# Kernel optimization log

Measured on AMD Instinct MI355X. Metric: run time of the kernel, lower is better.

Reference implementation:

```python
import jax, jax.numpy as jnp
import numpy as np

K = 3          # kernel size (implied by 18/27 offset channels)
PAD = 1
STRIDE = 1


def setup_inputs() -> dict:
    key = jax.random.key(0)
    k0, k1, k2 = jax.random.split(key, 3)
    B, C, H, W = 4, 256, 64, 64
    Cout = 256
    x = jax.random.normal(k0, (B, C, H, W), jnp.float32)
    # offset/mask predicting conv: 18 offset + 9 mask channels (deform_group=1)
    w_off = jax.random.normal(k1, (27, C, K, K), jnp.float32) * 0.01
    b_off = jnp.zeros((27,), jnp.float32)
    # main deformable conv weight (bias=False)
    w = jax.random.normal(k2, (Cout, C, K, K), jnp.float32) * 0.05
    return {"x": x, "w_off": w_off, "b_off": b_off, "w": w}


def _modulated_dcn(x, w_off, b_off, w):
    B, C, H, W = x.shape
    KK = K * K
    # regular conv predicting offsets (+ mask)
    om = jax.lax.conv_general_dilated(
        x, w_off, (STRIDE, STRIDE), [(PAD, PAD), (PAD, PAD)],
        dimension_numbers=("NCHW", "OIHW", "NCHW")) + b_off[None, :, None, None]
    Ho, Wo = om.shape[2], om.shape[3]
    # channel layout: interleaved (dy, dx) per kernel tap, then 9 mask channels
    off = om[:, :2 * KK].reshape(B, KK, 2, Ho, Wo)
    mask = jax.nn.sigmoid(om[:, 2 * KK:3 * KK])            # (B, KK, Ho, Wo)

    ky, kx = jnp.meshgrid(jnp.arange(K), jnp.arange(K), indexing="ij")
    base_y = (jnp.arange(Ho) * STRIDE - PAD)[:, None]       # (Ho, 1)
    base_x = (jnp.arange(Wo) * STRIDE - PAD)[None, :]       # (1, Wo)
    # sampling positions p = p0 + pn + offset, shape (B, KK, Ho, Wo)
    py = base_y[None, None] + ky.reshape(KK)[None, :, None, None] + off[:, :, 0]
    px = base_x[None, None] + kx.reshape(KK)[None, :, None, None] + off[:, :, 1]

    y0f = jnp.floor(py)
    x0f = jnp.floor(px)
    ly = py - y0f
    lx = px - x0f
    y0 = y0f.astype(jnp.int32)
    x0 = x0f.astype(jnp.int32)

    xf = x.reshape(B, C, H * W)

    def samp(yi, xi):
        valid = ((yi >= 0) & (yi < H) & (xi >= 0) & (xi < W)).astype(x.dtype)
        idx = jnp.clip(yi, 0, H - 1) * W + jnp.clip(xi, 0, W - 1)
        v = jnp.take_along_axis(xf, idx.reshape(B, 1, -1), axis=2)
        return v.reshape(B, C, KK, Ho, Wo) * valid[:, None]

    # bilinear interpolation with zero padding outside the image
    v = (samp(y0,     x0    ) * ((1 - ly) * (1 - lx))[:, None]
         + samp(y0,     x0 + 1) * ((1 - ly) * lx)[:, None]
         + samp(y0 + 1, x0    ) * (ly * (1 - lx))[:, None]
         + samp(y0 + 1, x0 + 1) * (ly * lx)[:, None])
    v = v * mask[:, None]                                   # modulation
    # conv as contraction over (Cin, KK)
    return jnp.einsum("bckhw,ock->bohw", v, w.reshape(w.shape[0], C, KK))


def reference(x, w_off, b_off, w):
    return _modulated_dcn(x, w_off, b_off, w)
```

## Files before the change

kernel.cpp:

```cpp
#include <hip/hip_runtime.h>
#include <math.h>

#define HH 64
#define WW 64
#define CIN 256
#define COUT 256
#define KKT 9
#define HWSZ 4096
#define VP 260

typedef __bf16  v8bf   __attribute__((ext_vector_type(8)));
typedef float   v4f    __attribute__((ext_vector_type(4)));
typedef short   short8 __attribute__((ext_vector_type(8)));
typedef unsigned short ushort4v __attribute__((ext_vector_type(4)));

__device__ inline unsigned short f2bf(float f) {
    union { float f; unsigned u; } uf; uf.f = f;
    unsigned r = uf.u + 0x7fff + ((uf.u >> 16) & 1);
    return (unsigned short)(r >> 16);
}
__device__ inline float bf2f(unsigned short u) {
    union { unsigned u; float f; } uf; uf.u = ((unsigned)u) << 16;
    return uf.f;
}

__global__ __launch_bounds__(256) void k_prep_x(const float* __restrict__ x,
                                                unsigned short* __restrict__ x_t) {
    int bh = blockIdx.x;
    int b  = bh >> 6;
    int h  = bh & 63;
    int px  = threadIdx.x & 63;
    int oct = threadIdx.x >> 6;
    const float* xr = x + (((size_t)b * CIN) * HH + h) * WW;
    unsigned short* orow = x_t + (((size_t)bh) * WW + px) * CIN;
    for (int g = 0; g < 8; g++) {
        int cb = g * 32 + oct * 8;
        unsigned short v[8];
#pragma unroll
        for (int j = 0; j < 8; j++)
            v[j] = f2bf(xr[(size_t)(cb + j) * HWSZ + px]);
        *(short8*)(orow + cb) = *(short8*)v;
    }
}

__global__ __launch_bounds__(256) void k_prep_wts(const float* __restrict__ w,
                                                  const float* __restrict__ w_off,
                                                  unsigned short* __restrict__ wprep,
                                                  unsigned short* __restrict__ woffp) {
    if (blockIdx.x < 256) {
        int o = blockIdx.x;
        for (int ck = threadIdx.x; ck < 2304; ck += 256) {
            float v = w[(size_t)o * 2304 + ck];
            int c  = ck / 9;
            int kk = ck - 9 * c;
            int kp = kk * 256 + c;
            wprep[((size_t)((kp >> 5) * 256 + o)) * 32 + (kp & 31)] = f2bf(v);
        }
    } else {
        int t = blockIdx.x - 256;
#pragma unroll
        for (int i = 0; i < 4; i++) {
            int idx = i * 256 + threadIdx.x;
            int och = idx >> 5;
            int ki  = idx & 31;
            int kp  = t * 32 + ki;
            int kk  = kp >> 8;
            int c   = kp & 255;
            float v = (och < 27) ? w_off[((size_t)och * 256 + c) * 9 + kk] : 0.f;
            woffp[(size_t)t * 1024 + idx] = f2bf(v);
        }
    }
}

__global__ __launch_bounds__(256) void k_off_mfma(const unsigned short* __restrict__ x_t,
                                                  const unsigned short* __restrict__ woffp,
                                                  const float* __restrict__ b_off,
                                                  float* __restrict__ om) {
    int id = blockIdx.x;
    int g  = id & 7, hi = (id >> 3) & 7, b = id >> 6;
    int h  = g * 8 + hi;
    int tid  = threadIdx.x;
    int lane = tid & 63;
    int wv   = tid >> 6;
    int m16  = lane & 15;
    int quad = lane >> 4;

    __shared__ unsigned short s_row[66 * VP];

    v4f acc[2];
    acc[0] = (v4f)(0.f);
    acc[1] = (v4f)(0.f);

    const unsigned short* xb = x_t + (size_t)b * HWSZ * CIN;

    if (tid < 64) {
        int hpx = (tid >> 5) * 65;
        int c8  = (tid & 31) * 8;
        *(short8*)&s_row[hpx * VP + c8] = (short8)0;
    }

    for (int ky = 0; ky < 3; ky++) {
        int y = h + ky - 1;
        __syncthreads();
        if ((unsigned)y < HH) {
            const unsigned short* src = xb + (size_t)y * WW * CIN;
#pragma unroll
            for (int i = 0; i < 8; i++) {
                int u  = i * 256 + tid;
                int px = u >> 5;
                int c8 = (u & 31) * 8;
                *(short8*)&s_row[(px + 1) * VP + c8] = *(const short8*)(src + px * CIN + c8);
            }
        } else {
#pragma unroll
            for (int i = 0; i < 8; i++) {
                int u  = i * 256 + tid;
                int px = u >> 5;
                int c8 = (u & 31) * 8;
                *(short8*)&s_row[(px + 1) * VP + c8] = (short8)0;
            }
        }
        __syncthreads();

#pragma unroll
        for (int kx = 0; kx < 3; kx++) {
            int kk = ky * 3 + kx;
#pragma unroll 4
            for (int ch = 0; ch < 8; ch++) {
                int t = kk * 8 + ch;
                const unsigned short* wp = woffp + (size_t)t * 1024;
                short8 af0 = *(const short8*)(wp + m16 * 32 + quad * 8);
                short8 af1 = *(const short8*)(wp + (16 + m16) * 32 + quad * 8);
                short8 bfr = *(const short8*)&s_row[(wv * 16 + m16 + kx) * VP + ch * 32 + quad * 8];
                acc[0] = __builtin_amdgcn_mfma_f32_16x16x32_bf16(
                    __builtin_bit_cast(v8bf, af0), __builtin_bit_cast(v8bf, bfr), acc[0], 0, 0, 0);
                acc[1] = __builtin_amdgcn_mfma_f32_16x16x32_bf16(
                    __builtin_bit_cast(v8bf, af1), __builtin_bit_cast(v8bf, bfr), acc[1], 0, 0, 0);
            }
        }
    }

#pragma unroll
    for (int mt = 0; mt < 2; mt++) {
#pragma unroll
        for (int r = 0; r < 4; r++) {
            int och = mt * 16 + quad * 4 + r;
            if (och < 27)
                om[((size_t)b * 27 + och) * HWSZ + h * WW + wv * 16 + m16] =
                    acc[mt][r] + b_off[och];
        }
    }
}

__global__ __launch_bounds__(512) void k_main(const unsigned short* __restrict__ x_t,
                                              const float* __restrict__ om,
                                              const unsigned short* __restrict__ wprep,
                                              float* __restrict__ out) {
    int id = blockIdx.x;
    int g  = id & 7, hi = (id >> 3) & 7, b = id >> 6;
    int h  = g * 8 + hi;
    int tid  = threadIdx.x;
    int lane = tid & 63;
    int oct  = tid >> 6;
    int m16  = lane & 15;
    int quad = lane >> 4;

    __shared__ int4   s_base[KKT][64];
    __shared__ float4 s_wt  [KKT][64];
    __shared__ unsigned short s_v[64 * VP];

    const float* omb = om + (size_t)b * 27 * HWSZ + h * WW;
    for (int i = tid; i < KKT * 64; i += 512) {
        int kk = i >> 6;
        int p  = i & 63;
        float offy = omb[(size_t)(2 * kk)     * HWSZ + p];
        float offx = omb[(size_t)(2 * kk + 1) * HWSZ + p];
        float mv   = omb[(size_t)(18 + kk)    * HWSZ + p];
        int ky = kk / 3, kx = kk - 3 * (kk / 3);
        float py = (float)(h - 1 + ky) + offy;
        float px = (float)(p - 1 + kx) + offx;
        float y0f = floorf(py);
        float x0f = floorf(px);
        float ly = py - y0f, lx = px - x0f;
        int y0 = (int)y0f, x0 = (int)x0f;
        float m = 1.f / (1.f + __expf(-mv));
        bool yv0 = (unsigned)y0       < HH;
        bool yv1 = (unsigned)(y0 + 1) < HH;
        bool xv0 = (unsigned)x0       < WW;
        bool xv1 = (unsigned)(x0 + 1) < WW;
        int y0c = min(max(y0, 0), HH - 1);
        int y1c = min(max(y0 + 1, 0), HH - 1);
        int x0c = min(max(x0, 0), WW - 1);
        int x1c = min(max(x0 + 1, 0), WW - 1);
        s_base[kk][p] = make_int4((y0c * WW + x0c) * CIN, (y0c * WW + x1c) * CIN,
                                  (y1c * WW + x0c) * CIN, (y1c * WW + x1c) * CIN);
        s_wt[kk][p] = make_float4(
            (yv0 && xv0) ? (1.f - ly) * (1.f - lx) * m : 0.f,
            (yv0 && xv1) ? (1.f - ly) * lx         * m : 0.f,
            (yv1 && xv0) ? ly * (1.f - lx)         * m : 0.f,
            (yv1 && xv1) ? ly * lx                 * m : 0.f);
    }
    __syncthreads();

    v4f acc[2][4];
#pragma unroll
    for (int mt = 0; mt < 2; mt++)
#pragma unroll
        for (int nt = 0; nt < 4; nt++) acc[mt][nt] = (v4f)(0.f);

    const unsigned short* xb = x_t + (size_t)b * HWSZ * CIN;

    for (int kk = 0; kk < KKT; kk++) {
#pragma unroll
        for (int i = 0; i < 8; i++) {
            int px = oct * 8 + i;
            int4   bp = s_base[kk][px];
            float4 wt = s_wt[kk][px];
            const unsigned short* xc = xb + lane * 4;
            ushort4v t0 = *(const ushort4v*)(xc + bp.x);
            ushort4v t1 = *(const ushort4v*)(xc + bp.y);
            ushort4v t2 = *(const ushort4v*)(xc + bp.z);
            ushort4v t3 = *(const ushort4v*)(xc + bp.w);
            unsigned short vv[4];
#pragma unroll
            for (int j = 0; j < 4; j++) {
                float val = wt.x * bf2f(t0[j]) + wt.y * bf2f(t1[j])
                          + wt.z * bf2f(t2[j]) + wt.w * bf2f(t3[j]);
                vv[j] = f2bf(val);
            }
            *(ushort4v*)&s_v[px * VP + lane * 4] = *(ushort4v*)vv;
        }
        __syncthreads();

#pragma unroll 2
        for (int ch = 0; ch < 8; ch++) {
            int t = kk * 8 + ch;
            const unsigned short* wp = wprep + ((size_t)t * 256 + oct * 32) * 32;
            short8 af0 = *(const short8*)(wp + m16 * 32 + quad * 8);
            short8 af1 = *(const short8*)(wp + (16 + m16) * 32 + quad * 8);
            short8 bfr[4];
#pragma unroll
            for (int nt = 0; nt < 4; nt++)
                bfr[nt] = *(const short8*)&s_v[(nt * 16 + m16) * VP + ch * 32 + quad * 8];
#pragma unroll
            for (int nt = 0; nt < 4; nt++) {
                acc[0][nt] = __builtin_amdgcn_mfma_f32_16x16x32_bf16(
                    __builtin_bit_cast(v8bf, af0), __builtin_bit_cast(v8bf, bfr[nt]),
                    acc[0][nt], 0, 0, 0);
                acc[1][nt] = __builtin_amdgcn_mfma_f32_16x16x32_bf16(
                    __builtin_bit_cast(v8bf, af1), __builtin_bit_cast(v8bf, bfr[nt]),
                    acc[1][nt], 0, 0, 0);
            }
        }
        __syncthreads();
    }

    float* ob = out + ((size_t)b * COUT) * HWSZ + h * WW;
#pragma unroll
    for (int mt = 0; mt < 2; mt++)
#pragma unroll
        for (int nt = 0; nt < 4; nt++)
#pragma unroll
            for (int r = 0; r < 4; r++) {
                int o = oct * 32 + mt * 16 + quad * 4 + r;
                ob[(size_t)o * HWSZ + nt * 16 + m16] = acc[mt][nt][r];
            }
}

extern "C" void kernel_launch(void* const* d_in, const int* in_sizes, int n_in,
                              void* d_out, int out_size, void* d_ws, size_t ws_size,
                              hipStream_t stream) {
    const float* x     = (const float*)d_in[0];
    const float* w_off = (const float*)d_in[1];
    const float* b_off = (const float*)d_in[2];
    const float* w     = (const float*)d_in[3];
    float* out = (float*)d_out;

    float* om = (float*)d_ws;
    unsigned short* x_t   = (unsigned short*)(om + 442368);
    unsigned short* wprep = x_t + (size_t)4 * HWSZ * CIN;
    unsigned short* woffp = wprep + 589824;

    hipLaunchKernelGGL(k_prep_x,   dim3(256), dim3(256), 0, stream, x, x_t);
    hipLaunchKernelGGL(k_prep_wts, dim3(328), dim3(256), 0, stream, w, w_off, wprep, woffp);
    hipLaunchKernelGGL(k_off_mfma, dim3(256), dim3(256), 0, stream, x_t, woffp, b_off, om);
    hipLaunchKernelGGL(k_main,     dim3(256), dim3(512), 0, stream, x_t, om, wprep, out);
}
```

Before: 156.6 us.

## Merge prep kernels, split offset conv, and double-buffer main gather with prefetch

Merges the x and weight prep kernels into one launch and stages w through shared memory, so the wprep writes become vectorized and coalesced. The offset conv now runs on 512 blocks, each covering half a row; all three input rows are loaded up front and the channel chunks are split across waves, with a shared-memory reduction at the end. The main kernel double-buffers the sampled tile and prefetches the next tap's gathered values and the next weight fragments into registers, which removes one barrier per tap. This costs more registers and more shared memory.

```diff
diff --git a/kernel.cpp b/kernel.cpp
--- a/kernel.cpp
+++ b/kernel.cpp
@@ -24,43 +24,52 @@
     return uf.f;
 }
 
-__global__ __launch_bounds__(256) void k_prep_x(const float* __restrict__ x,
-                                                unsigned short* __restrict__ x_t) {
-    int bh = blockIdx.x;
-    int b  = bh >> 6;
-    int h  = bh & 63;
-    int px  = threadIdx.x & 63;
-    int oct = threadIdx.x >> 6;
-    const float* xr = x + (((size_t)b * CIN) * HH + h) * WW;
-    unsigned short* orow = x_t + (((size_t)bh) * WW + px) * CIN;
-    for (int g = 0; g < 8; g++) {
-        int cb = g * 32 + oct * 8;
-        unsigned short v[8];
-#pragma unroll
-        for (int j = 0; j < 8; j++)
-            v[j] = f2bf(xr[(size_t)(cb + j) * HWSZ + px]);
-        *(short8*)(orow + cb) = *(short8*)v;
-    }
-}
-
-__global__ __launch_bounds__(256) void k_prep_wts(const float* __restrict__ w,
-                                                  const float* __restrict__ w_off,
-                                                  unsigned short* __restrict__ wprep,
-                                                  unsigned short* __restrict__ woffp) {
-    if (blockIdx.x < 256) {
-        int o = blockIdx.x;
-        for (int ck = threadIdx.x; ck < 2304; ck += 256) {
-            float v = w[(size_t)o * 2304 + ck];
-            int c  = ck / 9;
-            int kk = ck - 9 * c;
-            int kp = kk * 256 + c;
-            wprep[((size_t)((kp >> 5) * 256 + o)) * 32 + (kp & 31)] = f2bf(v);
+__global__ __launch_bounds__(256) void k_prep(const float* __restrict__ x,
+                                              const float* __restrict__ w,
+                                              const float* __restrict__ w_off,
+                                              unsigned short* __restrict__ x_t,
+                                              unsigned short* __restrict__ wprep,
+                                              unsigned short* __restrict__ woffp) {
+    __shared__ float s_w[2304];
+    int id  = blockIdx.x;
+    int tid = threadIdx.x;
+    if (id < 256) {
+        int b  = id >> 6;
+        int h  = id & 63;
+        int px  = tid & 63;
+        int oct = tid >> 6;
+        const float* xr = x + (((size_t)b * CIN) * HH + h) * WW;
+        unsigned short* orow = x_t + (((size_t)id) * WW + px) * CIN;
+        for (int g = 0; g < 8; g++) {
+            int cb = g * 32 + oct * 8;
+            unsigned short v[8];
+#pragma unroll
+            for (int j = 0; j < 8; j++)
+                v[j] = f2bf(xr[(size_t)(cb + j) * HWSZ + px]);
+            *(short8*)(orow + cb) = *(short8*)v;
+        }
+    } else if (id < 512) {
+        int o = id - 256;
+        for (int i = tid; i < 2304; i += 256) s_w[i] = w[(size_t)o * 2304 + i];
+        __syncthreads();
+        for (int u = tid; u < 576; u += 256) {
+            int t  = u >> 3;
+            int kq = u & 7;
+            unsigned short v[4];
+#pragma unroll
+            for (int j = 0; j < 4; j++) {
+                int kp = t * 32 + kq * 4 + j;
+                int kk = kp >> 8;
+                int c  = kp & 255;
+                v[j] = f2bf(s_w[c * 9 + kk]);
+            }
+            *(ushort4v*)&wprep[((size_t)(t * 256 + o)) * 32 + kq * 4] = *(ushort4v*)v;
         }
     } else {
-        int t = blockIdx.x - 256;
+        int t = id - 512;
 #pragma unroll
         for (int i = 0; i < 4; i++) {
-            int idx = i * 256 + threadIdx.x;
+            int idx = i * 256 + tid;
             int och = idx >> 5;
             int ki  = idx & 31;
             int kp  = t * 32 + ki;
@@ -76,62 +85,57 @@
                                                   const unsigned short* __restrict__ woffp,
                                                   const float* __restrict__ b_off,
                                                   float* __restrict__ om) {
-    int id = blockIdx.x;
-    int g  = id & 7, hi = (id >> 3) & 7, b = id >> 6;
-    int h  = g * 8 + hi;
+    int id    = blockIdx.x;
+    int g     = id & 7;
+    int phalf = (id >> 3) & 1;
+    int hi    = (id >> 4) & 7;
+    int b     = id >> 7;
+    int h     = g * 8 + hi;
+    int p0    = phalf * 32;
     int tid  = threadIdx.x;
     int lane = tid & 63;
     int wv   = tid >> 6;
+    int g2   = wv >> 1;
+    int ntw  = wv & 1;
     int m16  = lane & 15;
     int quad = lane >> 4;
 
-    __shared__ unsigned short s_row[66 * VP];
+    __shared__ unsigned short s_row[3 * 34 * VP];
+    __shared__ float s_red[2][32][33];
+
+    const unsigned short* xb = x_t + (size_t)b * HWSZ * CIN;
+
+    for (int u = tid; u < 3 * 1088; u += 256) {
+        int row = u / 1088;
+        int rem = u - row * 1088;
+        int px  = rem >> 5;
+        int c8  = (rem & 31) * 8;
+        int y   = h + row - 1;
+        int xg  = p0 + px - 1;
+        short8 val = (short8)0;
+        if ((unsigned)y < HH && (unsigned)xg < WW)
+            val = *(const short8*)(xb + ((size_t)y * WW + xg) * CIN + c8);
+        *(short8*)&s_row[(row * 34 + px) * VP + c8] = val;
+    }
+    __syncthreads();
 
     v4f acc[2];
     acc[0] = (v4f)(0.f);
     acc[1] = (v4f)(0.f);
 
-    const unsigned short* xb = x_t + (size_t)b * HWSZ * CIN;
-
-    if (tid < 64) {
-        int hpx = (tid >> 5) * 65;
-        int c8  = (tid & 31) * 8;
-        *(short8*)&s_row[hpx * VP + c8] = (short8)0;
-    }
-
+#pragma unroll
     for (int ky = 0; ky < 3; ky++) {
-        int y = h + ky - 1;
-        __syncthreads();
-        if ((unsigned)y < HH) {
-            const unsigned short* src = xb + (size_t)y * WW * CIN;
-#pragma unroll
-            for (int i = 0; i < 8; i++) {
-                int u  = i * 256 + tid;
-                int px = u >> 5;
-                int c8 = (u & 31) * 8;
-                *(short8*)&s_row[(px + 1) * VP + c8] = *(const short8*)(src + px * CIN + c8);
-            }
-        } else {
-#pragma unroll
-            for (int i = 0; i < 8; i++) {
-                int u  = i * 256 + tid;
-                int px = u >> 5;
-                int c8 = (u & 31) * 8;
-                *(short8*)&s_row[(px + 1) * VP + c8] = (short8)0;
-            }
-        }
-        __syncthreads();
-
 #pragma unroll
         for (int kx = 0; kx < 3; kx++) {
-            int kk = ky * 3 + kx;
-#pragma unroll 4
-            for (int ch = 0; ch < 8; ch++) {
-                int t = kk * 8 + ch;
+#pragma unroll
+            for (int c2 = 0; c2 < 4; c2++) {
+                int ch = c2 * 2 + g2;
+                int t  = (ky * 3 + kx) * 8 + ch;
                 const unsigned short* wp = woffp + (size_t)t * 1024;
                 short8 af0 = *(const short8*)(wp + m16 * 32 + quad * 8);
                 short8 af1 = *(const short8*)(wp + (16 + m16) * 32 + quad * 8);
-                short8 bfr = *(const short8*)&s_row[(wv * 16 + m16 + kx) * VP + ch * 32 + quad * 8];
+                short8 bfr = *(const short8*)
+                    &s_row[(ky * 34 + ntw * 16 + m16 + kx) * VP + ch * 32 + quad * 8];
                 acc[0] = __builtin_amdgcn_mfma_f32_16x16x32_bf16(
                     __builtin_bit_cast(v8bf, af0), __builtin_bit_cast(v8bf, bfr), acc[0], 0, 0, 0);
                 acc[1] = __builtin_amdgcn_mfma_f32_16x16x32_bf16(
@@ -141,21 +145,24 @@
     }
 
 #pragma unroll
-    for (int mt = 0; mt < 2; mt++) {
-#pragma unroll
-        for (int r = 0; r < 4; r++) {
-            int och = mt * 16 + quad * 4 + r;
-            if (och < 27)
-                om[((size_t)b * 27 + och) * HWSZ + h * WW + wv * 16 + m16] =
-                    acc[mt][r] + b_off[och];
-        }
-    }
-}
-
-__global__ __launch_bounds__(512) void k_main(const unsigned short* __restrict__ x_t,
-                                              const float* __restrict__ om,
-                                              const unsigned short* __restrict__ wprep,
-                                              float* __restrict__ out) {
+    for (int mt = 0; mt < 2; mt++)
+#pragma unroll
+        for (int r = 0; r < 4; r++)
+            s_red[g2][mt * 16 + quad * 4 + r][ntw * 16 + m16] = acc[mt][r];
+    __syncthreads();
+
+    for (int i2 = tid; i2 < 27 * 32; i2 += 256) {
+        int och = i2 >> 5;
+        int px  = i2 & 31;
+        float s = s_red[0][och][px] + s_red[1][och][px] + b_off[och];
+        om[((size_t)b * 27 + och) * HWSZ + h * WW + p0 + px] = s;
+    }
+}
+
+__global__ __launch_bounds__(512, 2) void k_main(const unsigned short* __restrict__ x_t,
+                                                 const float* __restrict__ om,
+                                                 const unsigned short* __restrict__ wprep,
+                                                 float* __restrict__ out) {
     int id = blockIdx.x;
     int g  = id & 7, hi = (id >> 3) & 7, b = id >> 6;
     int h  = g * 8 + hi;
@@ -167,7 +174,7 @@
 
     __shared__ int4   s_base[KKT][64];
     __shared__ float4 s_wt  [KKT][64];
-    __shared__ unsigned short s_v[64 * VP];
+    __shared__ unsigned short s_v[2][64 * VP];
 
     const float* omb = om + (size_t)b * 27 * HWSZ + h * WW;
     for (int i = tid; i < KKT * 64; i += 512) {
@@ -209,50 +216,74 @@
         for (int nt = 0; nt < 4; nt++) acc[mt][nt] = (v4f)(0.f);
 
     const unsigned short* xb = x_t + (size_t)b * HWSZ * CIN;
+    const unsigned short* xc = xb + lane * 4;
+
+    ushort4v vt[8][4];
+#pragma unroll
+    for (int i = 0; i < 8; i++) {
+        int4 bp = s_base[0][oct * 8 + i];
+        vt[i][0] = *(const ushort4v*)(xc + bp.x);
+        vt[i][1] = *(const ushort4v*)(xc + bp.y);
+        vt[i][2] = *(const ushort4v*)(xc + bp.z);
+        vt[i][3] = *(const ushort4v*)(xc + bp.w);
+    }
 
     for (int kk = 0; kk < KKT; kk++) {
+        unsigned short* vbuf = s_v[kk & 1];
+
 #pragma unroll
         for (int i = 0; i < 8; i++) {
             int px = oct * 8 + i;
-            int4   bp = s_base[kk][px];
             float4 wt = s_wt[kk][px];
-            const unsigned short* xc = xb + lane * 4;
-            ushort4v t0 = *(const ushort4v*)(xc + bp.x);
-            ushort4v t1 = *(const ushort4v*)(xc + bp.y);
-            ushort4v t2 = *(const ushort4v*)(xc + bp.z);
-            ushort4v t3 = *(const ushort4v*)(xc + bp.w);
             unsigned short vv[4];
 #pragma unroll
             for (int j = 0; j < 4; j++) {
-                float val = wt.x * bf2f(t0[j]) + wt.y * bf2f(t1[j])
-                          + wt.z * bf2f(t2[j]) + wt.w * bf2f(t3[j]);
+                float val = wt.x * bf2f(vt[i][0][j]) + wt.y * bf2f(vt[i][1][j])
+                          + wt.z * bf2f(vt[i][2][j]) + wt.w * bf2f(vt[i][3][j]);
                 vv[j] = f2bf(val);
             }
-            *(ushort4v*)&s_v[px * VP + lane * 4] = *(ushort4v*)vv;
+            *(ushort4v*)&vbuf[px * VP + lane * 4] = *(ushort4v*)vv;
         }
         __syncthreads();
 
-#pragma unroll 2
+        if (kk < KKT - 1) {
+#pragma unroll
+            for (int i = 0; i < 8; i++) {
+                int4 bp = s_base[kk + 1][oct * 8 + i];
+                vt[i][0] = *(const ushort4v*)(xc + bp.x);
+                vt[i][1] = *(const ushort4v*)(xc + bp.y);
+                vt[i][2] = *(const ushort4v*)(xc + bp.z);
+                vt[i][3] = *(const ushort4v*)(xc + bp.w);
+            }
+        }
+
+        int t0 = kk * 8;
+        const unsigned short* wp = wprep + ((size_t)t0 * 256 + oct * 32) * 32;
+        short8 wa0 = *(const short8*)(wp + m16 * 32 + quad * 8);
+        short8 wa1 = *(const short8*)(wp + (16 + m16) * 32 + quad * 8);
+#pragma unroll
         for (int ch = 0; ch < 8; ch++) {
-            int t = kk * 8 + ch;
-            const unsigned short* wp = wprep + ((size_t)t * 256 + oct * 32) * 32;
-            short8 af0 = *(const short8*)(wp + m16 * 32 + quad * 8);
-            short8 af1 = *(const short8*)(wp + (16 + m16) * 32 + quad * 8);
+            int tn = t0 + ch + 1;
+            if (tn > 71) tn = 71;
+            const unsigned short* wpn = wprep + ((size_t)tn * 256 + oct * 32) * 32;
+            short8 wn0 = *(const short8*)(wpn + m16 * 32 + quad * 8);
+            short8 wn1 = *(const short8*)(wpn + (16 + m16) * 32 + quad * 8);
             short8 bfr[4];
 #pragma unroll
             for (int nt = 0; nt < 4; nt++)
-                bfr[nt] = *(const short8*)&s_v[(nt * 16 + m16) * VP + ch * 32 + quad * 8];
+                bfr[nt] = *(const short8*)&vbuf[(nt * 16 + m16) * VP + ch * 32 + quad * 8];
 #pragma unroll
             for (int nt = 0; nt < 4; nt++) {
                 acc[0][nt] = __builtin_amdgcn_mfma_f32_16x16x32_bf16(
-                    __builtin_bit_cast(v8bf, af0), __builtin_bit_cast(v8bf, bfr[nt]),
+                    __builtin_bit_cast(v8bf, wa0), __builtin_bit_cast(v8bf, bfr[nt]),
                     acc[0][nt], 0, 0, 0);
                 acc[1][nt] = __builtin_amdgcn_mfma_f32_16x16x32_bf16(
-                    __builtin_bit_cast(v8bf, af1), __builtin_bit_cast(v8bf, bfr[nt]),
+                    __builtin_bit_cast(v8bf, wa1), __builtin_bit_cast(v8bf, bfr[nt]),
                     acc[1][nt], 0, 0, 0);
             }
-        }
-        __syncthreads();
+            wa0 = wn0;
+            wa1 = wn1;
+        }
     }
 
     float* ob = out + ((size_t)b * COUT) * HWSZ + h * WW;
@@ -281,8 +312,7 @@
     unsigned short* wprep = x_t + (size_t)4 * HWSZ * CIN;
     unsigned short* woffp = wprep + 589824;
 
-    hipLaunchKernelGGL(k_prep_x,   dim3(256), dim3(256), 0, stream, x, x_t);
-    hipLaunchKernelGGL(k_prep_wts, dim3(328), dim3(256), 0, stream, w, w_off, wprep, woffp);
-    hipLaunchKernelGGL(k_off_mfma, dim3(256), dim3(256), 0, stream, x_t, woffp, b_off, om);
+    hipLaunchKernelGGL(k_prep,     dim3(584), dim3(256), 0, stream, x, w, w_off, x_t, wprep, woffp);
+    hipLaunchKernelGGL(k_off_mfma, dim3(512), dim3(256), 0, stream, x_t, woffp, b_off, om);
     hipLaunchKernelGGL(k_main,     dim3(256), dim3(512), 0, stream, x_t, om, wprep, out);
 }
```

Measured after the change: 180.3 us. 15.2% more time.
